# Optimization experiments

Hardware: AMD Instinct MI355X
Metric: run time of the kernel (lower is better)

The kernel has to match this reference:

```python
import jax, jax.numpy as jnp
import numpy as np

DS = 4          # downsample_rate
BLOCKS = 3      # E2R blocks
EPS_REC = 1e-4  # SPDRectified eigenvalue floor (standard ReEig epsilon)
BN_EPS = 1e-5


def _patch_len(n, blocks):
    base = n // blocks
    ls = [base] * blocks
    for i in range(n - base * blocks):
        ls[i] += 1
    return ls


def _signal2spd(x):
    # x: (B, C, t) -> trace-normalized covariance + 1e-5 I, shape (B, C, C)
    x = x - x.mean(-1, keepdims=True)
    cov = jnp.einsum('bct,bdt->bcd', x, x) / (x.shape[-1] - 1)
    tra = jnp.trace(cov, axis1=-2, axis2=-1)[:, None, None]
    return cov / tra + 1e-5 * jnp.eye(cov.shape[-1], dtype=cov.dtype)


def setup_inputs() -> dict:
    key = jax.random.key(0)
    ks = jax.random.split(key, 6)
    bs, fb, chan, T = 256, 9, 22, 1000
    st, r, nc = 64, 32, 4
    x = jax.random.normal(ks[0], (bs, fb, chan, T), jnp.float32)
    conv_w = jax.random.normal(ks[1], (st, 1, chan, 13), jnp.float32) * 0.05
    conv_b = jnp.zeros((st,), jnp.float32)
    bn_gamma = jnp.ones((st,), jnp.float32)
    bn_beta = jnp.zeros((st,), jnp.float32)
    bn_mean = jnp.zeros((st,), jnp.float32)
    bn_var = jnp.ones((st,), jnp.float32)
    q, _ = jnp.linalg.qr(jax.random.normal(ks[2], (st, st), jnp.float32))
    bimap_w = q[:r].astype(jnp.float32)  # (r, st), semi-orthogonal Stiefel weight
    feat = fb * r * (r + 1) // 2
    linear_w = jax.random.normal(ks[3], (nc, feat), jnp.float32) * 0.02
    linear_b = jnp.zeros((nc,), jnp.float32)
    return dict(x=x, conv_w=conv_w, conv_b=conv_b, bn_gamma=bn_gamma,
                bn_beta=bn_beta, bn_mean=bn_mean, bn_var=bn_var,
                bimap_w=bimap_w, linear_w=linear_w, linear_b=linear_b)


def reference(x, conv_w, conv_b, bn_gamma, bn_beta, bn_mean, bn_var,
              bimap_w, linear_w, linear_b):
    bs, fb, chan, T = x.shape
    x = x.reshape(bs * fb, 1, chan, T)                   # freq bands folded into batch
    B = bs * fb
    Tp = T // DS
    x = x.reshape(B, 1, chan, Tp, DS).mean(-1)           # AvgPool2d((1, DS))
    x = jax.lax.conv_general_dilated(
        x, conv_w, (1, 1), ((0, 0), (6, 6)),
        dimension_numbers=('NCHW', 'OIHW', 'NCHW')) + conv_b[None, :, None, None]
    inv = bn_gamma / jnp.sqrt(bn_var + BN_EPS)           # eval-mode BatchNorm2d
    x = x * inv[None, :, None, None] + (bn_beta - bn_mean * inv)[None, :, None, None]
    x = x[:, :, 0, :]                                    # (B, st, Tp); H collapsed to 1

    # E2R: split time axis into BLOCKS (uneven allowed), covariance per block
    covs, off = [], 0
    for l in _patch_len(Tp, BLOCKS):
        covs.append(_signal2spd(x[..., off:off + l]))
        off += l
    cov = jnp.stack(covs, axis=1)                        # (B, blocks, st, st)

    # e_mean: BiMap W X W^T per block, then arithmetic mean over blocks
    y = jnp.einsum('oi,bmij,pj->bmop', bimap_w, cov, bimap_w).mean(axis=1)  # (B,r,r)

    # SPDRectified (ReEig): clamp eigenvalues
    s, u = jnp.linalg.eigh(y)
    y = jnp.einsum('bij,bj,bkj->bik', u, jnp.maximum(s, EPS_REC), u)

    # SPDTangentSpace: LogEig + upper-triangular vectorization (sqrt2 off-diag)
    s, u = jnp.linalg.eigh(y)
    logm = jnp.einsum('bij,bj,bkj->bik', u, jnp.log(s), u)
    r = logm.shape[-1]
    iu, ju = jnp.triu_indices(r)
    scale = jnp.where(iu == ju, 1.0, jnp.sqrt(2.0)).astype(logm.dtype)
    fe = logm[:, iu, ju] * scale                         # (B, r(r+1)/2)

    fe = fe.reshape(bs, -1)                              # (bs, fb * r(r+1)/2)
    logits = fe @ linear_w.T + linear_b
    return fe, logits
```

## Files before the change

kernel.cpp:

```cpp
#include <hip/hip_runtime.h>

#define B_TOT 2304
#define CHAN 22
#define TP 250
#define KW 13
#define ST 64
#define RANK 32
#define FE_PER 528
#define FE_TOTAL (B_TOT * FE_PER)
#define FEAT 4752
#define NC 4
#define NBS 256

__global__ __launch_bounds__(256) void ds_kernel(const float* __restrict__ x,
                                                 float* __restrict__ xds, int n) {
  int idx = blockIdx.x * 256 + threadIdx.x;
  if (idx < n) {
    float4 v = reinterpret_cast<const float4*>(x)[idx];
    xds[idx] = (v.x + v.y + v.z + v.w) * 0.25f;
  }
}

__global__ __launch_bounds__(256) void ccb_kernel(
    const float* __restrict__ xds, const float* __restrict__ conv_w,
    const float* __restrict__ conv_b, const float* __restrict__ bn_gamma,
    const float* __restrict__ bn_beta, const float* __restrict__ bn_mean,
    const float* __restrict__ bn_var, const float* __restrict__ bimap_w,
    float* __restrict__ ybuf) {
  const int b = blockIdx.x;
  const int m = blockIdx.y;
  const int off = (m == 0) ? 0 : (m == 1) ? 84 : 167;
  const int l = (m == 0) ? 84 : 83;
  const int tid = threadIdx.x;

  __shared__ union UU {
    struct {
      float xseg[CHAN][96];
      float wbuf[2][KW][ST];
    } s1;
    float Wlds[RANK][65];
  } u;
  __shared__ float S[ST][88];
  __shared__ float P[RANK][86];
  __shared__ float rowmean[ST];
  __shared__ float red4[4];

  const float* xb = xds + (size_t)b * CHAN * TP;
  for (int i = tid; i < CHAN * 96; i += 256) {
    int c = i / 96, tt = i - c * 96;
    int gt = off - 6 + tt;
    u.s1.xseg[c][tt] = (gt >= 0 && gt < TP) ? xb[c * TP + gt] : 0.0f;
  }
  for (int j = tid; j < KW * ST; j += 256) {
    int k = j >> 6, o = j & 63;
    u.s1.wbuf[0][k][o] = conv_w[o * (CHAN * KW) + 0 * KW + k];
  }
  __syncthreads();

  {
    const int og = tid >> 4, tg = tid & 15;
    const int o0 = og * 4, t0 = tg * 6;
    float acc[4][6];
#pragma unroll
    for (int a = 0; a < 4; a++)
#pragma unroll
      for (int t = 0; t < 6; t++) acc[a][t] = 0.f;

    for (int c = 0; c < CHAN; c++) {
      const int cur = c & 1;
      if (c + 1 < CHAN) {
        for (int j = tid; j < KW * ST; j += 256) {
          int k = j >> 6, o = j & 63;
          u.s1.wbuf[cur ^ 1][k][o] = conv_w[o * (CHAN * KW) + (c + 1) * KW + k];
        }
      }
      if (t0 < l) {
        float win[18];
#pragma unroll
        for (int j = 0; j < 18; j += 2) {
          float2 w2 = *reinterpret_cast<float2*>(&u.s1.xseg[c][t0 + j]);
          win[j] = w2.x; win[j + 1] = w2.y;
        }
#pragma unroll
        for (int k = 0; k < KW; k++) {
          float4 wv = *reinterpret_cast<float4*>(&u.s1.wbuf[cur][k][o0]);
#pragma unroll
          for (int t = 0; t < 6; t++) {
            float xv = win[k + t];
            acc[0][t] += wv.x * xv;
            acc[1][t] += wv.y * xv;
            acc[2][t] += wv.z * xv;
            acc[3][t] += wv.w * xv;
          }
        }
      }
      __syncthreads();
    }

    if (t0 < l) {
#pragma unroll
      for (int a = 0; a < 4; a++) {
        int o = o0 + a;
        float inv = bn_gamma[o] * rsqrtf(bn_var[o] + 1e-5f);
        float shift = bn_beta[o] - bn_mean[o] * inv;
        float bias = conv_b[o];
#pragma unroll
        for (int t = 0; t < 6; t++) {
          int tt = t0 + t;
          if (tt < l) S[o][tt] = (acc[a][t] + bias) * inv + shift;
        }
      }
    }
  }
  __syncthreads();

  {
    int row = tid >> 2, part = tid & 3;
    float ssum = 0.f;
    for (int t = part; t < l; t += 4) ssum += S[row][t];
    ssum += __shfl_xor(ssum, 1);
    ssum += __shfl_xor(ssum, 2);
    if (part == 0) rowmean[row] = ssum / (float)l;
  }
  __syncthreads();

  float ssq_loc = 0.f;
  for (int i = tid; i < ST * 84; i += 256) {
    int o = i / 84, t = i - o * 84;
    if (t < l) {
      float v = S[o][t] - rowmean[o];
      S[o][t] = v;
      ssq_loc += v * v;
    }
  }
  for (int j = tid; j < RANK * ST; j += 256) {
    u.Wlds[j >> 6][j & 63] = bimap_w[j];
  }
#pragma unroll
  for (int d = 32; d >= 1; d >>= 1) ssq_loc += __shfl_xor(ssq_loc, d);
  if ((tid & 63) == 0) red4[tid >> 6] = ssq_loc;
  __syncthreads();
  const float ssq = red4[0] + red4[1] + red4[2] + red4[3];

  {
    const int po = tid >> 4;
    const int ptg = tid & 15;
    const int t0p = ptg * 6;
    if (t0p < l) {
      float pacc[2][6];
#pragma unroll
      for (int a = 0; a < 2; a++)
#pragma unroll
        for (int t = 0; t < 6; t++) pacc[a][t] = 0.f;
      for (int i = 0; i < ST; i++) {
        float w0 = u.Wlds[2 * po][i];
        float w1 = u.Wlds[2 * po + 1][i];
        float sv[6];
#pragma unroll
        for (int j = 0; j < 6; j += 2) {
          float2 s2 = *reinterpret_cast<float2*>(&S[i][t0p + j]);
          sv[j] = s2.x; sv[j + 1] = s2.y;
        }
#pragma unroll
        for (int t = 0; t < 6; t++) {
          pacc[0][t] += w0 * sv[t];
          pacc[1][t] += w1 * sv[t];
        }
      }
#pragma unroll
      for (int a = 0; a < 2; a++)
#pragma unroll
        for (int t = 0; t < 6; t++) {
          int tt = t0p + t;
          if (tt < l) P[2 * po + a][tt] = pacc[a][t];
        }
    }
  }
  __syncthreads();

  {
    const int ty = tid >> 4;
    const int tx = tid & 15;
    const int r0 = 2 * ty, c0 = 2 * tx;
    float ya = 0.f, yb_ = 0.f, yc = 0.f, yd = 0.f;
    int t = 0;
    for (; t + 1 < l; t += 2) {
      float2 a0 = *reinterpret_cast<float2*>(&P[r0][t]);
      float2 a1 = *reinterpret_cast<float2*>(&P[r0 + 1][t]);
      float2 b0 = *reinterpret_cast<float2*>(&P[c0][t]);
      float2 b1 = *reinterpret_cast<float2*>(&P[c0 + 1][t]);
      ya += a0.x * b0.x + a0.y * b0.y;
      yb_ += a0.x * b1.x + a0.y * b1.y;
      yc += a1.x * b0.x + a1.y * b0.y;
      yd += a1.x * b1.x + a1.y * b1.y;
    }
    if (t < l) {
      float a0 = P[r0][t], a1 = P[r0 + 1][t], b0 = P[c0][t], b1 = P[c0 + 1][t];
      ya += a0 * b0; yb_ += a0 * b1; yc += a1 * b0; yd += a1 * b1;
    }
    const float sy = 1.0f / (3.0f * ssq);
    const float dg = 1e-5f / 3.0f;
    float* yp = ybuf + (size_t)(b * 3 + m) * RANK * RANK;
    yp[r0 * RANK + c0]           = ya * sy + ((r0 == c0) ? dg : 0.f);
    yp[r0 * RANK + c0 + 1]       = yb_ * sy;
    yp[(r0 + 1) * RANK + c0]     = yc * sy;
    yp[(r0 + 1) * RANK + c0 + 1] = yd * sy + ((r0 + 1 == c0 + 1) ? dg : 0.f);
  }
}

__global__ __launch_bounds__(256) void eig_kernel(const float* __restrict__ ybuf,
                                                  float* __restrict__ feout) {
  int b = blockIdx.x;
  int tid = threadIdx.x;
  __shared__ float A[32][33];
  __shared__ float V[32][33];
  __shared__ float cs[16], sn[16];
  __shared__ int pp[16], qq[16];
  __shared__ float lam[32];
  __shared__ float redo[4], redf[4];

  const float* yb = ybuf + (size_t)b * 3 * 1024;
  for (int i = tid; i < 1024; i += 256) {
    int r = i >> 5, c = i & 31;
    float v = yb[i] + yb[1024 + i] + yb[2048 + i];
    int it = c * 32 + r;
    float vt = yb[it] + yb[1024 + it] + yb[2048 + it];
    A[r][c] = 0.5f * (v + vt);
    V[r][c] = (r == c) ? 1.0f : 0.0f;
  }

  for (int sw = 0; sw < 12; sw++) {
    __syncthreads();
    float loc = 0.f, frol = 0.f;
    for (int i = tid; i < 1024; i += 256) {
      int r = i >> 5, c = i & 31;
      float v = A[r][c];
      frol += v * v;
      if (r != c) loc += v * v;
    }
#pragma unroll
    for (int d = 32; d >= 1; d >>= 1) {
      loc += __shfl_xor(loc, d);
      frol += __shfl_xor(frol, d);
    }
    if ((tid & 63) == 0) { redo[tid >> 6] = loc; redf[tid >> 6] = frol; }
    __syncthreads();
    float offn = redo[0] + redo[1] + redo[2] + redo[3];
    float fro2 = redf[0] + redf[1] + redf[2] + redf[3];
    if (offn <= 1e-13f * fro2) break;

    for (int rr = 0; rr < 31; rr++) {
      __syncthreads();
      if (tid < 16) {
        int p, q;
        if (tid == 0) { p = 31; q = rr; }
        else { p = (rr + tid) % 31; q = (rr + 31 - tid) % 31; }
        float app = A[p][p], aqq = A[q][q], apq = A[p][q];
        float c, s;
        if (fabsf(apq) < 1e-30f) { c = 1.f; s = 0.f; }
        else {
          float tau = (aqq - app) / (2.f * apq);
          float t = copysignf(1.f, tau) / (fabsf(tau) + sqrtf(1.f + tau * tau));
          c = rsqrtf(1.f + t * t);
          s = t * c;
        }
        cs[tid] = c; sn[tid] = s; pp[tid] = p; qq[tid] = q;
      }
      __syncthreads();
      for (int it = tid; it < 512; it += 256) {
        int k = it >> 5, col = it & 31;
        int p = pp[k], q = qq[k];
        float c = cs[k], s = sn[k];
        float ap = A[p][col], aq = A[q][col];
        A[p][col] = c * ap - s * aq;
        A[q][col] = s * ap + c * aq;
      }
      __syncthreads();
      for (int it = tid; it < 1024; it += 256) {
        int k = (it >> 5) & 15;
        int row = it & 31;
        int p = pp[k], q = qq[k];
        float c = cs[k], s = sn[k];
        if (it < 512) {
          float ap = A[row][p], aq = A[row][q];
          A[row][p] = c * ap - s * aq;
          A[row][q] = s * ap + c * aq;
        } else {
          float vp = V[row][p], vq = V[row][q];
          V[row][p] = c * vp - s * vq;
          V[row][q] = s * vp + c * vq;
        }
      }
    }
  }
  __syncthreads();

  if (tid < 32) lam[tid] = logf(fmaxf(A[tid][tid], 1e-4f));
  __syncthreads();

  for (int idx = tid; idx < FE_PER; idx += 256) {
    int i = 0, rem = idx;
    while (rem >= 32 - i) { rem -= 32 - i; i++; }
    int j = i + rem;
    float acc = 0.f;
#pragma unroll
    for (int k = 0; k < 32; k++) acc += V[i][k] * lam[k] * V[j][k];
    float scalef = (i == j) ? 1.0f : 1.4142135623730951f;
    feout[(size_t)b * FE_PER + idx] = acc * scalef;
  }
}

__global__ __launch_bounds__(256) void logits_kernel(const float* __restrict__ fe,
                                                     const float* __restrict__ lw,
                                                     const float* __restrict__ lb,
                                                     float* __restrict__ outp) {
  int bs = blockIdx.x, tid = threadIdx.x;
  const float* f = fe + (size_t)bs * FEAT;
  float acc[NC] = {0.f, 0.f, 0.f, 0.f};
  for (int i = tid; i < FEAT; i += 256) {
    float v = f[i];
#pragma unroll
    for (int c = 0; c < NC; c++) acc[c] += v * lw[c * FEAT + i];
  }
  __shared__ float partial[4][NC];
#pragma unroll
  for (int c = 0; c < NC; c++) {
    float v = acc[c];
#pragma unroll
    for (int d = 32; d >= 1; d >>= 1) v += __shfl_xor(v, d);
    acc[c] = v;
  }
  if ((tid & 63) == 0) {
    int wave = tid >> 6;
#pragma unroll
    for (int c = 0; c < NC; c++) partial[wave][c] = acc[c];
  }
  __syncthreads();
  if (tid == 0) {
#pragma unroll
    for (int c = 0; c < NC; c++) {
      float sum = partial[0][c] + partial[1][c] + partial[2][c] + partial[3][c];
      outp[bs * NC + c] = sum + lb[c];
    }
  }
}

extern "C" void kernel_launch(void* const* d_in, const int* in_sizes, int n_in,
                              void* d_out, int out_size, void* d_ws, size_t ws_size,
                              hipStream_t stream) {
  const float* x        = (const float*)d_in[0];
  const float* conv_w   = (const float*)d_in[1];
  const float* conv_b   = (const float*)d_in[2];
  const float* bn_gamma = (const float*)d_in[3];
  const float* bn_beta  = (const float*)d_in[4];
  const float* bn_mean  = (const float*)d_in[5];
  const float* bn_var   = (const float*)d_in[6];
  const float* bimap_w  = (const float*)d_in[7];
  const float* linear_w = (const float*)d_in[8];
  const float* linear_b = (const float*)d_in[9];
  float* out = (float*)d_out;

  float* xds  = (float*)d_ws;
  float* ybuf = xds + 12672000;

  int n = B_TOT * CHAN * TP;
  ds_kernel<<<(n + 255) / 256, 256, 0, stream>>>(x, xds, n);

  dim3 g2(B_TOT, 3);
  ccb_kernel<<<g2, 256, 0, stream>>>(xds, conv_w, conv_b, bn_gamma, bn_beta,
                                     bn_mean, bn_var, bimap_w, ybuf);

  eig_kernel<<<B_TOT, 256, 0, stream>>>(ybuf, out);

  logits_kernel<<<NBS, 256, 0, stream>>>(out, linear_w, linear_b, out + FE_TOTAL);
}
```

Baseline: 1.300 ms.

## Run Jacobi eigensolver in one wavefront and prefold BatchNorm into conv weights

The eigen kernel now runs one 64-lane wavefront per matrix. Each group of 4 lanes computes its own rotation for a Jacobi pair and applies the row and column updates with float4 LDS accesses, using wave barriers in place of block-wide __syncthreads. A new pre-kernel folds the BatchNorm scale into transposed conv weights and a fused bias, so the conv kernel loads contiguous float4 weight slices. The log-eig reconstruction also prescales V by the log eigenvalues. The risks are a fourfold drop in threads per eig block and reliance on wave-level ordering of LDS writes between the row and column phases.

After: 1.253 ms. -3.6%, faster.

```diff
diff --git a/kernel.cpp b/kernel.cpp
--- a/kernel.cpp
+++ b/kernel.cpp
@@ -11,6 +11,7 @@
 #define FEAT 4752
 #define NC 4
 #define NBS 256
+#define WTN (CHAN * KW * ST)
 
 __global__ __launch_bounds__(256) void ds_kernel(const float* __restrict__ x,
                                                  float* __restrict__ xds, int n) {
@@ -21,11 +22,28 @@
   }
 }
 
+__global__ __launch_bounds__(256) void wt_kernel(
+    const float* __restrict__ conv_w, const float* __restrict__ conv_b,
+    const float* __restrict__ bn_gamma, const float* __restrict__ bn_beta,
+    const float* __restrict__ bn_mean, const float* __restrict__ bn_var,
+    float* __restrict__ wt, float* __restrict__ bias_eff) {
+  int idx = blockIdx.x * 256 + threadIdx.x;
+  if (idx < WTN) {
+    int c = idx / (KW * ST);
+    int rem = idx - c * (KW * ST);
+    int k = rem >> 6, o = rem & 63;
+    float inv = bn_gamma[o] * rsqrtf(bn_var[o] + 1e-5f);
+    wt[idx] = conv_w[o * (CHAN * KW) + c * KW + k] * inv;
+  } else if (idx < WTN + ST) {
+    int o = idx - WTN;
+    float inv = bn_gamma[o] * rsqrtf(bn_var[o] + 1e-5f);
+    bias_eff[o] = conv_b[o] * inv + bn_beta[o] - bn_mean[o] * inv;
+  }
+}
+
 __global__ __launch_bounds__(256) void ccb_kernel(
-    const float* __restrict__ xds, const float* __restrict__ conv_w,
-    const float* __restrict__ conv_b, const float* __restrict__ bn_gamma,
-    const float* __restrict__ bn_beta, const float* __restrict__ bn_mean,
-    const float* __restrict__ bn_var, const float* __restrict__ bimap_w,
+    const float* __restrict__ xds, const float* __restrict__ wt,
+    const float* __restrict__ bias_eff, const float* __restrict__ bimap_w,
     float* __restrict__ ybuf) {
   const int b = blockIdx.x;
   const int m = blockIdx.y;
@@ -36,7 +54,7 @@
   __shared__ union UU {
     struct {
       float xseg[CHAN][96];
-      float wbuf[2][KW][ST];
+      float wbuf[2][KW * ST];
     } s1;
     float Wlds[RANK][65];
   } u;
@@ -51,9 +69,9 @@
     int gt = off - 6 + tt;
     u.s1.xseg[c][tt] = (gt >= 0 && gt < TP) ? xb[c * TP + gt] : 0.0f;
   }
-  for (int j = tid; j < KW * ST; j += 256) {
-    int k = j >> 6, o = j & 63;
-    u.s1.wbuf[0][k][o] = conv_w[o * (CHAN * KW) + 0 * KW + k];
+  if (tid < 208) {
+    float4 w4 = reinterpret_cast<const float4*>(wt)[tid];
+    *reinterpret_cast<float4*>(&u.s1.wbuf[0][tid * 4]) = w4;
   }
   __syncthreads();
 
@@ -68,11 +86,9 @@
 
     for (int c = 0; c < CHAN; c++) {
       const int cur = c & 1;
-      if (c + 1 < CHAN) {
-        for (int j = tid; j < KW * ST; j += 256) {
-          int k = j >> 6, o = j & 63;
-          u.s1.wbuf[cur ^ 1][k][o] = conv_w[o * (CHAN * KW) + (c + 1) * KW + k];
-        }
+      if (c + 1 < CHAN && tid < 208) {
+        float4 w4 = reinterpret_cast<const float4*>(wt + (size_t)(c + 1) * (KW * ST))[tid];
+        *reinterpret_cast<float4*>(&u.s1.wbuf[cur ^ 1][tid * 4]) = w4;
       }
       if (t0 < l) {
         float win[18];
@@ -83,7 +99,7 @@
         }
 #pragma unroll
         for (int k = 0; k < KW; k++) {
-          float4 wv = *reinterpret_cast<float4*>(&u.s1.wbuf[cur][k][o0]);
+          float4 wv = *reinterpret_cast<float4*>(&u.s1.wbuf[cur][k * 64 + o0]);
 #pragma unroll
           for (int t = 0; t < 6; t++) {
             float xv = win[k + t];
@@ -101,13 +117,11 @@
 #pragma unroll
       for (int a = 0; a < 4; a++) {
         int o = o0 + a;
-        float inv = bn_gamma[o] * rsqrtf(bn_var[o] + 1e-5f);
-        float shift = bn_beta[o] - bn_mean[o] * inv;
-        float bias = conv_b[o];
+        float be = bias_eff[o];
 #pragma unroll
         for (int t = 0; t < 6; t++) {
           int tt = t0 + t;
-          if (tt < l) S[o][tt] = (acc[a][t] + bias) * inv + shift;
+          if (tt < l) S[o][tt] = acc[a][t] + be;
         }
       }
     }
@@ -204,23 +218,20 @@
     yp[r0 * RANK + c0]           = ya * sy + ((r0 == c0) ? dg : 0.f);
     yp[r0 * RANK + c0 + 1]       = yb_ * sy;
     yp[(r0 + 1) * RANK + c0]     = yc * sy;
-    yp[(r0 + 1) * RANK + c0 + 1] = yd * sy + ((r0 + 1 == c0 + 1) ? dg : 0.f);
-  }
-}
-
-__global__ __launch_bounds__(256) void eig_kernel(const float* __restrict__ ybuf,
-                                                  float* __restrict__ feout) {
-  int b = blockIdx.x;
-  int tid = threadIdx.x;
-  __shared__ float A[32][33];
-  __shared__ float V[32][33];
-  __shared__ float cs[16], sn[16];
-  __shared__ int pp[16], qq[16];
+    yp[(r0 + 1) * RANK + c0 + 1] = yd * sy + dg;
+  }
+}
+
+__global__ __launch_bounds__(64) void eig_kernel(const float* __restrict__ ybuf,
+                                                 float* __restrict__ feout) {
+  const int b = blockIdx.x;
+  const int lane = threadIdx.x;
+  __shared__ float A[32][36];
+  __shared__ float V[32][36];
   __shared__ float lam[32];
-  __shared__ float redo[4], redf[4];
-
-  const float* yb = ybuf + (size_t)b * 3 * 1024;
-  for (int i = tid; i < 1024; i += 256) {
+
+  const float* yb = ybuf + (size_t)b * 3072;
+  for (int i = lane; i < 1024; i += 64) {
     int r = i >> 5, c = i & 31;
     float v = yb[i] + yb[1024 + i] + yb[2048 + i];
     int it = c * 32 + r;
@@ -228,83 +239,96 @@
     A[r][c] = 0.5f * (v + vt);
     V[r][c] = (r == c) ? 1.0f : 0.0f;
   }
+  __syncthreads();
+
+  const int k = lane >> 2;
+  const int sub = lane & 3;
+  const int c8 = 8 * sub;
 
   for (int sw = 0; sw < 12; sw++) {
-    __syncthreads();
-    float loc = 0.f, frol = 0.f;
-    for (int i = tid; i < 1024; i += 256) {
+    float loc = 0.f, fro = 0.f;
+    for (int i = lane; i < 1024; i += 64) {
       int r = i >> 5, c = i & 31;
       float v = A[r][c];
-      frol += v * v;
+      fro += v * v;
       if (r != c) loc += v * v;
     }
 #pragma unroll
     for (int d = 32; d >= 1; d >>= 1) {
       loc += __shfl_xor(loc, d);
-      frol += __shfl_xor(frol, d);
-    }
-    if ((tid & 63) == 0) { redo[tid >> 6] = loc; redf[tid >> 6] = frol; }
-    __syncthreads();
-    float offn = redo[0] + redo[1] + redo[2] + redo[3];
-    float fro2 = redf[0] + redf[1] + redf[2] + redf[3];
-    if (offn <= 1e-13f * fro2) break;
+      fro += __shfl_xor(fro, d);
+    }
+    if (loc <= 1e-13f * fro) break;
 
     for (int rr = 0; rr < 31; rr++) {
-      __syncthreads();
-      if (tid < 16) {
-        int p, q;
-        if (tid == 0) { p = 31; q = rr; }
-        else { p = (rr + tid) % 31; q = (rr + 31 - tid) % 31; }
-        float app = A[p][p], aqq = A[q][q], apq = A[p][q];
-        float c, s;
-        if (fabsf(apq) < 1e-30f) { c = 1.f; s = 0.f; }
-        else {
-          float tau = (aqq - app) / (2.f * apq);
-          float t = copysignf(1.f, tau) / (fabsf(tau) + sqrtf(1.f + tau * tau));
-          c = rsqrtf(1.f + t * t);
-          s = t * c;
-        }
-        cs[tid] = c; sn[tid] = s; pp[tid] = p; qq[tid] = q;
+      int p, q;
+      if (k == 0) { p = 31; q = rr; }
+      else { p = (rr + k) % 31; q = (rr + 31 - k) % 31; }
+
+      float app = A[p][p], aqq = A[q][q], apq = A[p][q];
+      bool tiny = fabsf(apq) < 1e-30f;
+      float apq_s = tiny ? 1.0f : apq;
+      float tau = (aqq - app) / (2.f * apq_s);
+      float t = copysignf(1.f, tau) / (fabsf(tau) + sqrtf(1.f + tau * tau));
+      float c_ = rsqrtf(1.f + t * t);
+      float s_ = t * c_;
+      c_ = tiny ? 1.f : c_;
+      s_ = tiny ? 0.f : s_;
+
+      float4 rp0 = *reinterpret_cast<float4*>(&A[p][c8]);
+      float4 rp1 = *reinterpret_cast<float4*>(&A[p][c8 + 4]);
+      float4 rq0 = *reinterpret_cast<float4*>(&A[q][c8]);
+      float4 rq1 = *reinterpret_cast<float4*>(&A[q][c8 + 4]);
+      float4 np0, np1, nq0, nq1;
+      np0.x = c_ * rp0.x - s_ * rq0.x;  nq0.x = s_ * rp0.x + c_ * rq0.x;
+      np0.y = c_ * rp0.y - s_ * rq0.y;  nq0.y = s_ * rp0.y + c_ * rq0.y;
+      np0.z = c_ * rp0.z - s_ * rq0.z;  nq0.z = s_ * rp0.z + c_ * rq0.z;
+      np0.w = c_ * rp0.w - s_ * rq0.w;  nq0.w = s_ * rp0.w + c_ * rq0.w;
+      np1.x = c_ * rp1.x - s_ * rq1.x;  nq1.x = s_ * rp1.x + c_ * rq1.x;
+      np1.y = c_ * rp1.y - s_ * rq1.y;  nq1.y = s_ * rp1.y + c_ * rq1.y;
+      np1.z = c_ * rp1.z - s_ * rq1.z;  nq1.z = s_ * rp1.z + c_ * rq1.z;
+      np1.w = c_ * rp1.w - s_ * rq1.w;  nq1.w = s_ * rp1.w + c_ * rq1.w;
+      *reinterpret_cast<float4*>(&A[p][c8])     = np0;
+      *reinterpret_cast<float4*>(&A[p][c8 + 4]) = np1;
+      *reinterpret_cast<float4*>(&A[q][c8])     = nq0;
+      *reinterpret_cast<float4*>(&A[q][c8 + 4]) = nq1;
+      __builtin_amdgcn_wave_barrier();
+
+#pragma unroll
+      for (int j = 0; j < 8; j++) {
+        int row = c8 + j;
+        float ap = A[row][p], aq = A[row][q];
+        A[row][p] = c_ * ap - s_ * aq;
+        A[row][q] = s_ * ap + c_ * aq;
+        float vp = V[row][p], vq = V[row][q];
+        V[row][p] = c_ * vp - s_ * vq;
+        V[row][q] = s_ * vp + c_ * vq;
       }
-      __syncthreads();
-      for (int it = tid; it < 512; it += 256) {
-        int k = it >> 5, col = it & 31;
-        int p = pp[k], q = qq[k];
-        float c = cs[k], s = sn[k];
-        float ap = A[p][col], aq = A[q][col];
-        A[p][col] = c * ap - s * aq;
-        A[q][col] = s * ap + c * aq;
-      }
-      __syncthreads();
-      for (int it = tid; it < 1024; it += 256) {
-        int k = (it >> 5) & 15;
-        int row = it & 31;
-        int p = pp[k], q = qq[k];
-        float c = cs[k], s = sn[k];
-        if (it < 512) {
-          float ap = A[row][p], aq = A[row][q];
-          A[row][p] = c * ap - s * aq;
-          A[row][q] = s * ap + c * aq;
-        } else {
-          float vp = V[row][p], vq = V[row][q];
-          V[row][p] = c * vp - s * vq;
-          V[row][q] = s * vp + c * vq;
-        }
-      }
-    }
-  }
-  __syncthreads();
-
-  if (tid < 32) lam[tid] = logf(fmaxf(A[tid][tid], 1e-4f));
-  __syncthreads();
-
-  for (int idx = tid; idx < FE_PER; idx += 256) {
+      __builtin_amdgcn_wave_barrier();
+    }
+  }
+  __syncthreads();
+
+  if (lane < 32) lam[lane] = logf(fmaxf(A[lane][lane], 1e-4f));
+  __syncthreads();
+
+  for (int i = lane; i < 1024; i += 64) {
+    int r = i >> 5, c = i & 31;
+    A[r][c] = V[r][c] * lam[c];
+  }
+  __syncthreads();
+
+  for (int idx = lane; idx < FE_PER; idx += 64) {
     int i = 0, rem = idx;
     while (rem >= 32 - i) { rem -= 32 - i; i++; }
     int j = i + rem;
     float acc = 0.f;
 #pragma unroll
-    for (int k = 0; k < 32; k++) acc += V[i][k] * lam[k] * V[j][k];
+    for (int kk = 0; kk < 32; kk += 4) {
+      float4 av = *reinterpret_cast<float4*>(&A[i][kk]);
+      float4 vv = *reinterpret_cast<float4*>(&V[j][kk]);
+      acc += av.x * vv.x + av.y * vv.y + av.z * vv.z + av.w * vv.w;
+    }
     float scalef = (i == j) ? 1.0f : 1.4142135623730951f;
     feout[(size_t)b * FE_PER + idx] = acc * scalef;
   }
@@ -360,17 +384,21 @@
   const float* linear_b = (const float*)d_in[9];
   float* out = (float*)d_out;
 
-  float* xds  = (float*)d_ws;
-  float* ybuf = xds + 12672000;
+  float* xds      = (float*)d_ws;
+  float* ybuf     = xds + 12672000;
+  float* wt       = ybuf + 7077888;
+  float* bias_eff = wt + WTN;
+
+  wt_kernel<<<(WTN + ST + 255) / 256, 256, 0, stream>>>(
+      conv_w, conv_b, bn_gamma, bn_beta, bn_mean, bn_var, wt, bias_eff);
 
   int n = B_TOT * CHAN * TP;
   ds_kernel<<<(n + 255) / 256, 256, 0, stream>>>(x, xds, n);
 
   dim3 g2(B_TOT, 3);
-  ccb_kernel<<<g2, 256, 0, stream>>>(xds, conv_w, conv_b, bn_gamma, bn_beta,
-                                     bn_mean, bn_var, bimap_w, ybuf);
-
-  eig_kernel<<<B_TOT, 256, 0, stream>>>(ybuf, out);
+  ccb_kernel<<<g2, 256, 0, stream>>>(xds, wt, bias_eff, bimap_w, ybuf);
+
+  eig_kernel<<<B_TOT, 64, 0, stream>>>(ybuf, out);
 
   logits_kernel<<<NBS, 256, 0, stream>>>(out, linear_w, linear_b, out + FE_TOTAL);
 }
```
